# Optimization experiments

Measured on AMD Instinct MI355X. Metric: run time of the kernel, lower is better.

Reference implementation:

```python
import jax, jax.numpy as jnp
import numpy as np

B = 256   # batch size; must equal N for the module's final broadcast to be valid
N = 256   # num feature vectors per sample
D = 1024  # feature dim
S = 1024  # state dim


def setup_inputs() -> dict:
    key = jax.random.key(0)
    k1, k2, k3, k4 = jax.random.split(key, 4)
    return {
        "feature_vectors": jax.random.normal(k1, (B, N, D), dtype=jnp.float32),
        "state_output": jax.random.normal(k2, (B, S), dtype=jnp.float32),
        # tf.random_normal_initializer default stddev=0.05
        "Q": 0.05 * jax.random.normal(k3, (S, S), dtype=jnp.float32),
        "K": 0.05 * jax.random.normal(k4, (S, N), dtype=jnp.float32),
    }


def reference(feature_vectors, state_output, Q, K):
    # Loop body: ((Q @ state^T)^T @ K) @ feature_vectors[i]
    # (Q @ state^T)^T == state @ Q^T  -> [B, S]
    A = state_output @ Q.T            # [B, S]
    M = A @ K                         # [B, N]
    # stack over i: W[i, b, d] = sum_n M[b, n] * FV[i, n, d]
    W = jnp.einsum('bn,ind->ibd', M, feature_vectors)   # [B, B, D]
    W = jax.nn.softmax(W, axis=-1)
    # broadcast multiply [B, B, D] * [B, N(=B), D], sum over axis=1
    context_vector = jnp.sum(W * feature_vectors, axis=1)  # [B, D]
    return (context_vector, W)
```

## Files before the change

### kernel.cpp

```cpp
#include <hip/hip_runtime.h>


typedef _Float16 half8 __attribute__((ext_vector_type(8)));
typedef float floatx16 __attribute__((ext_vector_type(16)));

static __device__ __forceinline__ void split_f32(float x, _Float16& hi, _Float16& lo) {
    _Float16 h = (_Float16)x;
    hi = h;
    lo = (_Float16)(x - (float)h);
}

template <bool BT>
__global__ __launch_bounds__(256, 2) void gemm_splitk(
    const float* __restrict__ Ag, const float* __restrict__ Bg,
    float* __restrict__ Cf, int Kdim, int Ndim, int KC)
{
    __shared__ __align__(16) _Float16 AsHi[4 * 64 * 8];
    __shared__ __align__(16) _Float16 AsLo[4 * 64 * 8];
    __shared__ __align__(16) _Float16 BsHi[4 * 64 * 8];
    __shared__ __align__(16) _Float16 BsLo[4 * 64 * 8];

    const int tid  = threadIdx.x;
    const int lane = tid & 63;
    const int wave = tid >> 6;
    const int wy = wave >> 1, wx = wave & 1;
    const int l31 = lane & 31, l5 = lane >> 5;
    const int m0 = blockIdx.y * 64, n0 = blockIdx.x * 64;
    const int kt0 = (blockIdx.z * KC) >> 5;

    floatx16 acc;
#pragma unroll
    for (int j = 0; j < 16; ++j) acc[j] = 0.0f;

    const int sA_m  = tid >> 2;
    const int sA_kg = tid & 3;
    const int sB_n  = tid & 63;
    const int sB_kg = tid >> 6;

    const int nkt = KC / 32;
#pragma unroll 1
    for (int kt2 = 0; kt2 < nkt; ++kt2) {
        const int kt = kt0 + kt2;
        __syncthreads();
        {
            const float* src = Ag + (size_t)(m0 + sA_m) * Kdim + kt * 32 + sA_kg * 8;
            half8 hi, lo;
#pragma unroll
            for (int j = 0; j < 8; ++j) {
                _Float16 h, l;
                split_f32(src[j], h, l);
                hi[j] = h; lo[j] = l;
            }
            *(half8*)&AsHi[(sA_kg * 64 + sA_m) * 8] = hi;
            *(half8*)&AsLo[(sA_kg * 64 + sA_m) * 8] = lo;
        }
        if constexpr (BT) {
            const float* src = Bg + (size_t)(n0 + sA_m) * Kdim + kt * 32 + sA_kg * 8;
            half8 hi, lo;
#pragma unroll
            for (int j = 0; j < 8; ++j) {
                _Float16 h, l;
                split_f32(src[j], h, l);
                hi[j] = h; lo[j] = l;
            }
            *(half8*)&BsHi[(sA_kg * 64 + sA_m) * 8] = hi;
            *(half8*)&BsLo[(sA_kg * 64 + sA_m) * 8] = lo;
        } else {
            const float* src = Bg + (size_t)(kt * 32 + sB_kg * 8) * Ndim + n0 + sB_n;
            half8 hi, lo;
#pragma unroll
            for (int j = 0; j < 8; ++j) {
                _Float16 h, l;
                split_f32(src[(size_t)j * Ndim], h, l);
                hi[j] = h; lo[j] = l;
            }
            *(half8*)&BsHi[(sB_kg * 64 + sB_n) * 8] = hi;
            *(half8*)&BsLo[(sB_kg * 64 + sB_n) * 8] = lo;
        }
        __syncthreads();
#pragma unroll
        for (int ks = 0; ks < 2; ++ks) {
            const int kg = ks * 2 + l5;
            const half8 ah = *(half8*)&AsHi[(kg * 64 + wy * 32 + l31) * 8];
            const half8 al = *(half8*)&AsLo[(kg * 64 + wy * 32 + l31) * 8];
            const half8 bh = *(half8*)&BsHi[(kg * 64 + wx * 32 + l31) * 8];
            const half8 bl = *(half8*)&BsLo[(kg * 64 + wx * 32 + l31) * 8];
            acc = __builtin_amdgcn_mfma_f32_32x32x16_f16(ah, bh, acc, 0, 0, 0);
            acc = __builtin_amdgcn_mfma_f32_32x32x16_f16(ah, bl, acc, 0, 0, 0);
            acc = __builtin_amdgcn_mfma_f32_32x32x16_f16(al, bh, acc, 0, 0, 0);
        }
    }

#pragma unroll
    for (int reg = 0; reg < 16; ++reg) {
        const int row = m0 + wy * 32 + (reg & 3) + 8 * (reg >> 2) + 4 * l5;
        const int col = n0 + wx * 32 + l31;
        atomicAdd(&Cf[(size_t)row * Ndim + col], acc[reg]);
    }
}

static __device__ __forceinline__ int bs_swz(int byte_off) {
    return byte_off ^ (((byte_off >> 7) & 7) << 4);
}

__global__ __launch_bounds__(512, 2) void fused_attn(
    const float* __restrict__ FV, const float* __restrict__ Mf,
    float* __restrict__ ctx, float* __restrict__ Wout)
{
    __shared__ __align__(16) _Float16 AsHi[2 * 64 * 8];
    __shared__ __align__(16) _Float16 AsLo[2 * 64 * 8];
    __shared__ __align__(16) _Float16 Bs[2 * 1024 * 8];
    __shared__ __align__(16) float red1[64 * 4];
    __shared__ __align__(16) float red2[64 * 4];

    const int tid  = threadIdx.x;
    const int lane = tid & 63;
    const int wave = tid >> 6;
    const int wx = wave & 3;
    const int wy = wave >> 2;
    const int l31 = lane & 31, l5 = lane >> 5;

    const int w   = blockIdx.x;
    const int xcd = w & 7;
    const int k   = w >> 3;
    const int i   = (xcd << 5) + (k >> 2);
    const int bt  = k & 3;

    const float* __restrict__ FVi = FV + (size_t)i * 256 * 1024;

    floatx16 acc[8];
#pragma unroll
    for (int nt = 0; nt < 8; ++nt)
#pragma unroll
        for (int j = 0; j < 16; ++j) acc[nt][j] = 0.0f;

    const int am = tid >> 1, akg = tid & 1;

    const int n8 = tid >> 8;
    const int c0 = (tid & 255) * 4;

    float4 pv4[8];
    float4 pa0, pa1;
    {
        const float* src = FVi + (size_t)(n8 * 8) * 1024 + c0;
#pragma unroll
        for (int r = 0; r < 8; ++r) pv4[r] = *(const float4*)(src + (size_t)r * 1024);
    }
    if (tid < 128) {
        const float* ap = Mf + (size_t)(bt * 64 + am) * 256 + akg * 8;
        pa0 = *(const float4*)(ap);
        pa1 = *(const float4*)(ap + 4);
    }

#pragma unroll 1
    for (int kt = 0; kt < 16; ++kt) {
        __syncthreads();
        if (tid < 128) {
            half8 hi, lo;
#pragma unroll
            for (int j = 0; j < 4; ++j) {
                _Float16 h, l;
                split_f32((&pa0.x)[j], h, l);
                hi[j] = h; lo[j] = l;
            }
#pragma unroll
            for (int j = 0; j < 4; ++j) {
                _Float16 h, l;
                split_f32((&pa1.x)[j], h, l);
                hi[4 + j] = h; lo[4 + j] = l;
            }
            *(half8*)&AsHi[(akg * 64 + am) * 8] = hi;
            *(half8*)&AsLo[(akg * 64 + am) * 8] = lo;
        }
#pragma unroll
        for (int j = 0; j < 4; ++j) {
            half8 h;
#pragma unroll
            for (int r = 0; r < 8; ++r) h[r] = (_Float16)((&pv4[r].x)[j]);
            const int byte_off = (n8 * 1024 + c0 + j) * 16;
            *(half8*)((char*)Bs + bs_swz(byte_off)) = h;
        }
        __syncthreads();
        if (kt + 1 < 16) {
            const float* src = FVi + (size_t)((kt + 1) * 16 + n8 * 8) * 1024 + c0;
#pragma unroll
            for (int r = 0; r < 8; ++r) pv4[r] = *(const float4*)(src + (size_t)r * 1024);
            if (tid < 128) {
                const float* ap = Mf + (size_t)(bt * 64 + am) * 256 + (kt + 1) * 16 + akg * 8;
                pa0 = *(const float4*)(ap);
                pa1 = *(const float4*)(ap + 4);
            }
        }
        const half8 ah = *(half8*)&AsHi[(l5 * 64 + wy * 32 + l31) * 8];
        const half8 al = *(half8*)&AsLo[(l5 * 64 + wy * 32 + l31) * 8];
#pragma unroll
        for (int nt = 0; nt < 8; ++nt) {
            const int byte_off = (l5 * 1024 + wx * 256 + nt * 32 + l31) * 16;
            const half8 b = *(const half8*)((const char*)Bs + bs_swz(byte_off));
            acc[nt] = __builtin_amdgcn_mfma_f32_32x32x16_f16(ah, b, acc[nt], 0, 0, 0);
            acc[nt] = __builtin_amdgcn_mfma_f32_32x32x16_f16(al, b, acc[nt], 0, 0, 0);
        }
    }

    float st[16];
#pragma unroll
    for (int reg = 0; reg < 16; ++reg) {
        float v = acc[0][reg];
#pragma unroll
        for (int nt = 1; nt < 8; ++nt) v = fmaxf(v, acc[nt][reg]);
#pragma unroll
        for (int off = 1; off < 32; off <<= 1) v = fmaxf(v, __shfl_xor(v, off));
        st[reg] = v;
    }
    if (l31 == 0) {
#pragma unroll
        for (int reg = 0; reg < 16; ++reg) {
            const int row = wy * 32 + (reg & 3) + 8 * (reg >> 2) + 4 * l5;
            red1[row * 4 + wx] = st[reg];
        }
    }
    __syncthreads();
    float rmax[16];
#pragma unroll
    for (int reg = 0; reg < 16; ++reg) {
        const int row = wy * 32 + (reg & 3) + 8 * (reg >> 2) + 4 * l5;
        const float4 m4 = *(const float4*)&red1[row * 4];
        rmax[reg] = fmaxf(fmaxf(m4.x, m4.y), fmaxf(m4.z, m4.w));
    }
#pragma unroll
    for (int reg = 0; reg < 16; ++reg) {
        float s = 0.0f;
#pragma unroll
        for (int nt = 0; nt < 8; ++nt) {
            const float p = __expf(acc[nt][reg] - rmax[reg]);
            acc[nt][reg] = p;
            s += p;
        }
#pragma unroll
        for (int off = 1; off < 32; off <<= 1) s += __shfl_xor(s, off);
        st[reg] = s;
    }
    if (l31 == 0) {
#pragma unroll
        for (int reg = 0; reg < 16; ++reg) {
            const int row = wy * 32 + (reg & 3) + 8 * (reg >> 2) + 4 * l5;
            red2[row * 4 + wx] = st[reg];
        }
    }
    __syncthreads();
    float inv[16];
#pragma unroll
    for (int reg = 0; reg < 16; ++reg) {
        const int row = wy * 32 + (reg & 3) + 8 * (reg >> 2) + 4 * l5;
        const float4 s4 = *(const float4*)&red2[row * 4];
        inv[reg] = 1.0f / (s4.x + s4.y + s4.z + s4.w);
    }

    float csum[8];
#pragma unroll
    for (int nt = 0; nt < 8; ++nt) csum[nt] = 0.0f;

    const int rowbase = bt * 64 + wy * 32;
#pragma unroll
    for (int nt = 0; nt < 8; ++nt) {
        const int col = wx * 256 + nt * 32 + l31;
#pragma unroll
        for (int reg = 0; reg < 16; ++reg) {
            const int row = (reg & 3) + 8 * (reg >> 2) + 4 * l5;
            const float wv = acc[nt][reg] * inv[reg];
            Wout[((size_t)(i * 256 + rowbase + row)) * 1024 + col] = wv;
            const float fv = FVi[(size_t)(rowbase + row) * 1024 + col];
            csum[nt] += wv * fv;
        }
    }
#pragma unroll
    for (int nt = 0; nt < 8; ++nt) {
        const float v = csum[nt] + __shfl_xor(csum[nt], 32);
        if (l5 == 0)
            atomicAdd(&ctx[(size_t)i * 1024 + wx * 256 + nt * 32 + l31], v);
    }
}

extern "C" void kernel_launch(void* const* d_in, const int* in_sizes, int n_in,
                              void* d_out, int out_size, void* d_ws, size_t ws_size,
                              hipStream_t stream)
{
    const float* FV    = (const float*)d_in[0];
    const float* state = (const float*)d_in[1];
    const float* Q     = (const float*)d_in[2];
    const float* Km    = (const float*)d_in[3];

    float* out = (float*)d_out;
    float* ctx = out;
    float* W   = out + 256 * 1024;

    char* ws = (char*)d_ws;
    float* A1 = (float*)ws;
    float* Mf = (float*)(ws + (1 << 20));

    (void)hipMemsetAsync(ws, 0, (1 << 20) + (1 << 18), stream);
    (void)hipMemsetAsync(ctx, 0, 256 * 1024 * sizeof(float), stream);

    gemm_splitk<true><<<dim3(16, 4, 8), 256, 0, stream>>>(
        state, Q, A1, 1024, 1024, 128);

    gemm_splitk<false><<<dim3(4, 4, 16), 256, 0, stream>>>(
        A1, Km, Mf, 1024, 256, 64);

    fused_attn<<<dim3(1024), 512, 0, stream>>>(FV, Mf, ctx, W);
}
```

Measured before the change: 588.0 us.

## Double fused attention block to 1024 threads with 16 waves and smaller per-wave tiles

```diff
diff --git a/kernel.cpp b/kernel.cpp
--- a/kernel.cpp
+++ b/kernel.cpp
@@ -2,6 +2,7 @@
 
 
 typedef _Float16 half8 __attribute__((ext_vector_type(8)));
+typedef _Float16 half4 __attribute__((ext_vector_type(4)));
 typedef float floatx16 __attribute__((ext_vector_type(16)));
 
 static __device__ __forceinline__ void split_f32(float x, _Float16& hi, _Float16& lo) {
@@ -103,21 +104,21 @@
     return byte_off ^ (((byte_off >> 7) & 7) << 4);
 }
 
-__global__ __launch_bounds__(512, 2) void fused_attn(
+__global__ __launch_bounds__(1024, 4) void fused_attn(
     const float* __restrict__ FV, const float* __restrict__ Mf,
     float* __restrict__ ctx, float* __restrict__ Wout)
 {
     __shared__ __align__(16) _Float16 AsHi[2 * 64 * 8];
     __shared__ __align__(16) _Float16 AsLo[2 * 64 * 8];
     __shared__ __align__(16) _Float16 Bs[2 * 1024 * 8];
-    __shared__ __align__(16) float red1[64 * 4];
-    __shared__ __align__(16) float red2[64 * 4];
+    __shared__ __align__(16) float red1[64 * 8];
+    __shared__ __align__(16) float red2[64 * 8];
 
     const int tid  = threadIdx.x;
     const int lane = tid & 63;
     const int wave = tid >> 6;
-    const int wx = wave & 3;
-    const int wy = wave >> 2;
+    const int wx = wave & 7;
+    const int wy = wave >> 3;
     const int l31 = lane & 31, l5 = lane >> 5;
 
     const int w   = blockIdx.x;
@@ -128,24 +129,22 @@
 
     const float* __restrict__ FVi = FV + (size_t)i * 256 * 1024;
 
-    floatx16 acc[8];
-#pragma unroll
-    for (int nt = 0; nt < 8; ++nt)
+    floatx16 acc[4];
+#pragma unroll
+    for (int nt = 0; nt < 4; ++nt)
 #pragma unroll
         for (int j = 0; j < 16; ++j) acc[nt][j] = 0.0f;
 
     const int am = tid >> 1, akg = tid & 1;
 
-    const int n8 = tid >> 8;
-    const int c0 = (tid & 255) * 4;
-
-    float4 pv4[8];
+    const int ng = tid >> 8;
+    const int dq = tid & 255;
+
+    float4 pv[4];
     float4 pa0, pa1;
-    {
-        const float* src = FVi + (size_t)(n8 * 8) * 1024 + c0;
-#pragma unroll
-        for (int r = 0; r < 8; ++r) pv4[r] = *(const float4*)(src + (size_t)r * 1024);
-    }
+#pragma unroll
+    for (int r = 0; r < 4; ++r)
+        pv[r] = *(const float4*)(FVi + (size_t)(ng * 4 + r) * 1024 + dq * 4);
     if (tid < 128) {
         const float* ap = Mf + (size_t)(bt * 64 + am) * 256 + akg * 8;
         pa0 = *(const float4*)(ap);
@@ -174,17 +173,17 @@
         }
 #pragma unroll
         for (int j = 0; j < 4; ++j) {
-            half8 h;
-#pragma unroll
-            for (int r = 0; r < 8; ++r) h[r] = (_Float16)((&pv4[r].x)[j]);
-            const int byte_off = (n8 * 1024 + c0 + j) * 16;
-            *(half8*)((char*)Bs + bs_swz(byte_off)) = h;
+            half4 h;
+#pragma unroll
+            for (int r = 0; r < 4; ++r) h[r] = (_Float16)((&pv[r].x)[j]);
+            const int byte_off = ((ng >> 1) * 1024 + dq * 4 + j) * 16 + (ng & 1) * 8;
+            *(half4*)((char*)Bs + bs_swz(byte_off)) = h;
         }
         __syncthreads();
         if (kt + 1 < 16) {
-            const float* src = FVi + (size_t)((kt + 1) * 16 + n8 * 8) * 1024 + c0;
-#pragma unroll
-            for (int r = 0; r < 8; ++r) pv4[r] = *(const float4*)(src + (size_t)r * 1024);
+#pragma unroll
+            for (int r = 0; r < 4; ++r)
+                pv[r] = *(const float4*)(FVi + (size_t)((kt + 1) * 16 + ng * 4 + r) * 1024 + dq * 4);
             if (tid < 128) {
                 const float* ap = Mf + (size_t)(bt * 64 + am) * 256 + (kt + 1) * 16 + akg * 8;
                 pa0 = *(const float4*)(ap);
@@ -194,90 +193,72 @@
         const half8 ah = *(half8*)&AsHi[(l5 * 64 + wy * 32 + l31) * 8];
         const half8 al = *(half8*)&AsLo[(l5 * 64 + wy * 32 + l31) * 8];
 #pragma unroll
-        for (int nt = 0; nt < 8; ++nt) {
-            const int byte_off = (l5 * 1024 + wx * 256 + nt * 32 + l31) * 16;
+        for (int nt = 0; nt < 4; ++nt) {
+            const int byte_off = (l5 * 1024 + wx * 128 + nt * 32 + l31) * 16;
             const half8 b = *(const half8*)((const char*)Bs + bs_swz(byte_off));
             acc[nt] = __builtin_amdgcn_mfma_f32_32x32x16_f16(ah, b, acc[nt], 0, 0, 0);
             acc[nt] = __builtin_amdgcn_mfma_f32_32x32x16_f16(al, b, acc[nt], 0, 0, 0);
         }
     }
 
-    float st[16];
 #pragma unroll
     for (int reg = 0; reg < 16; ++reg) {
         float v = acc[0][reg];
 #pragma unroll
-        for (int nt = 1; nt < 8; ++nt) v = fmaxf(v, acc[nt][reg]);
+        for (int nt = 1; nt < 4; ++nt) v = fmaxf(v, acc[nt][reg]);
 #pragma unroll
         for (int off = 1; off < 32; off <<= 1) v = fmaxf(v, __shfl_xor(v, off));
-        st[reg] = v;
-    }
-    if (l31 == 0) {
-#pragma unroll
-        for (int reg = 0; reg < 16; ++reg) {
+        if (l31 == 0) {
             const int row = wy * 32 + (reg & 3) + 8 * (reg >> 2) + 4 * l5;
-            red1[row * 4 + wx] = st[reg];
+            red1[row * 8 + wx] = v;
         }
     }
     __syncthreads();
-    float rmax[16];
 #pragma unroll
     for (int reg = 0; reg < 16; ++reg) {
         const int row = wy * 32 + (reg & 3) + 8 * (reg >> 2) + 4 * l5;
-        const float4 m4 = *(const float4*)&red1[row * 4];
-        rmax[reg] = fmaxf(fmaxf(m4.x, m4.y), fmaxf(m4.z, m4.w));
-    }
-#pragma unroll
-    for (int reg = 0; reg < 16; ++reg) {
+        const float4 a4 = *(const float4*)&red1[row * 8];
+        const float4 b4 = *(const float4*)&red1[row * 8 + 4];
+        const float rmax = fmaxf(fmaxf(fmaxf(a4.x, a4.y), fmaxf(a4.z, a4.w)),
+                                 fmaxf(fmaxf(b4.x, b4.y), fmaxf(b4.z, b4.w)));
         float s = 0.0f;
 #pragma unroll
-        for (int nt = 0; nt < 8; ++nt) {
-            const float p = __expf(acc[nt][reg] - rmax[reg]);
+        for (int nt = 0; nt < 4; ++nt) {
+            const float p = __expf(acc[nt][reg] - rmax);
             acc[nt][reg] = p;
             s += p;
         }
 #pragma unroll
         for (int off = 1; off < 32; off <<= 1) s += __shfl_xor(s, off);
-        st[reg] = s;
-    }
-    if (l31 == 0) {
-#pragma unroll
-        for (int reg = 0; reg < 16; ++reg) {
-            const int row = wy * 32 + (reg & 3) + 8 * (reg >> 2) + 4 * l5;
-            red2[row * 4 + wx] = st[reg];
-        }
+        if (l31 == 0) red2[row * 8 + wx] = s;
     }
     __syncthreads();
-    float inv[16];
-#pragma unroll
-    for (int reg = 0; reg < 16; ++reg) {
-        const int row = wy * 32 + (reg & 3) + 8 * (reg >> 2) + 4 * l5;
-        const float4 s4 = *(const float4*)&red2[row * 4];
-        inv[reg] = 1.0f / (s4.x + s4.y + s4.z + s4.w);
-    }
-
-    float csum[8];
-#pragma unroll
-    for (int nt = 0; nt < 8; ++nt) csum[nt] = 0.0f;
+
+    float csum[4];
+#pragma unroll
+    for (int nt = 0; nt < 4; ++nt) csum[nt] = 0.0f;
 
     const int rowbase = bt * 64 + wy * 32;
 #pragma unroll
-    for (int nt = 0; nt < 8; ++nt) {
-        const int col = wx * 256 + nt * 32 + l31;
-#pragma unroll
-        for (int reg = 0; reg < 16; ++reg) {
-            const int row = (reg & 3) + 8 * (reg >> 2) + 4 * l5;
-            const float wv = acc[nt][reg] * inv[reg];
+    for (int reg = 0; reg < 16; ++reg) {
+        const int row = (reg & 3) + 8 * (reg >> 2) + 4 * l5;
+        const float4 a4 = *(const float4*)&red2[(wy * 32 + row) * 8];
+        const float4 b4 = *(const float4*)&red2[(wy * 32 + row) * 8 + 4];
+        const float inv = 1.0f / (a4.x + a4.y + a4.z + a4.w + b4.x + b4.y + b4.z + b4.w);
+#pragma unroll
+        for (int nt = 0; nt < 4; ++nt) {
+            const int col = wx * 128 + nt * 32 + l31;
+            const float wv = acc[nt][reg] * inv;
             Wout[((size_t)(i * 256 + rowbase + row)) * 1024 + col] = wv;
             const float fv = FVi[(size_t)(rowbase + row) * 1024 + col];
             csum[nt] += wv * fv;
         }
     }
 #pragma unroll
-    for (int nt = 0; nt < 8; ++nt) {
+    for (int nt = 0; nt < 4; ++nt) {
         const float v = csum[nt] + __shfl_xor(csum[nt], 32);
         if (l5 == 0)
-            atomicAdd(&ctx[(size_t)i * 1024 + wx * 256 + nt * 32 + l31], v);
+            atomicAdd(&ctx[(size_t)i * 1024 + wx * 128 + nt * 32 + l31], v);
     }
 }
 
@@ -307,5 +288,5 @@
     gemm_splitk<false><<<dim3(4, 4, 16), 256, 0, stream>>>(
         A1, Km, Mf, 1024, 256, 64);
 
-    fused_attn<<<dim3(1024), 512, 0, stream>>>(FV, Mf, ctx, W);
-}
+    fused_attn<<<dim3(1024), 1024, 0, stream>>>(FV, Mf, ctx, W);
+}
```

New measurement: 585.7 us. Within noise of the previous version (-0.4%).

## Pre-convert feature vectors to fp16 in a pass fused with the first GEMM

Applied to the files above, without the earlier changes.

```diff
diff --git a/kernel.cpp b/kernel.cpp
--- a/kernel.cpp
+++ b/kernel.cpp
@@ -2,6 +2,7 @@
 
 
 typedef _Float16 half8 __attribute__((ext_vector_type(8)));
+typedef _Float16 half4 __attribute__((ext_vector_type(4)));
 typedef float floatx16 __attribute__((ext_vector_type(16)));
 
 static __device__ __forceinline__ void split_f32(float x, _Float16& hi, _Float16& lo) {
@@ -10,10 +11,10 @@
     lo = (_Float16)(x - (float)h);
 }
 
-template <bool BT>
-__global__ __launch_bounds__(256, 2) void gemm_splitk(
+template <bool BT, bool SPLITK>
+__device__ __forceinline__ void gemm_body(
     const float* __restrict__ Ag, const float* __restrict__ Bg,
-    float* __restrict__ Cf, int Kdim, int Ndim, int KC)
+    float* __restrict__ Cf, int Kdim, int Ndim, int KC, int bx, int by, int bz)
 {
     __shared__ __align__(16) _Float16 AsHi[4 * 64 * 8];
     __shared__ __align__(16) _Float16 AsLo[4 * 64 * 8];
@@ -25,8 +26,8 @@
     const int wave = tid >> 6;
     const int wy = wave >> 1, wx = wave & 1;
     const int l31 = lane & 31, l5 = lane >> 5;
-    const int m0 = blockIdx.y * 64, n0 = blockIdx.x * 64;
-    const int kt0 = (blockIdx.z * KC) >> 5;
+    const int m0 = by * 64, n0 = bx * 64;
+    const int kt0 = (bz * KC) >> 5;
 
     floatx16 acc;
 #pragma unroll
@@ -95,8 +96,47 @@
     for (int reg = 0; reg < 16; ++reg) {
         const int row = m0 + wy * 32 + (reg & 3) + 8 * (reg >> 2) + 4 * l5;
         const int col = n0 + wx * 32 + l31;
-        atomicAdd(&Cf[(size_t)row * Ndim + col], acc[reg]);
-    }
+        if constexpr (SPLITK) atomicAdd(&Cf[(size_t)row * Ndim + col], acc[reg]);
+        else                  Cf[(size_t)row * Ndim + col] = acc[reg];
+    }
+}
+
+template <bool BT>
+__global__ __launch_bounds__(256, 2) void gemm_splitk(
+    const float* __restrict__ Ag, const float* __restrict__ Bg,
+    float* __restrict__ Cf, int Kdim, int Ndim, int KC)
+{
+    gemm_body<BT, true>(Ag, Bg, Cf, Kdim, Ndim, KC,
+                        blockIdx.x, blockIdx.y, blockIdx.z);
+}
+
+__device__ __forceinline__ void fv16_copy_body(
+    const float* __restrict__ FV, _Float16* __restrict__ T, int i, int tile, int z)
+{
+    const size_t base = (size_t)i * 262144 + (size_t)tile * 16384 + (size_t)z * 2048;
+    const float* src = FV + base;
+    _Float16* dst = T + base;
+    const int tid = threadIdx.x;
+#pragma unroll
+    for (int j = 0; j < 2; ++j) {
+        const float4 v = *(const float4*)(src + (size_t)(j * 256 + tid) * 4);
+        half4 h;
+        h[0] = (_Float16)v.x; h[1] = (_Float16)v.y;
+        h[2] = (_Float16)v.z; h[3] = (_Float16)v.w;
+        *(half4*)(dst + (size_t)(j * 256 + tid) * 4) = h;
+    }
+}
+
+__global__ __launch_bounds__(256, 2) void gemm1_plus_copy(
+    const float* __restrict__ state, const float* __restrict__ Q,
+    float* __restrict__ A1,
+    const float* __restrict__ FV, _Float16* __restrict__ T)
+{
+    if (blockIdx.y < 4)
+        gemm_body<true, true>(state, Q, A1, 1024, 1024, 128,
+                              blockIdx.x, blockIdx.y, blockIdx.z);
+    else
+        fv16_copy_body(FV, T, blockIdx.y - 4, blockIdx.x, blockIdx.z);
 }
 
 static __device__ __forceinline__ int bs_swz(int byte_off) {
@@ -104,7 +144,7 @@
 }
 
 __global__ __launch_bounds__(512, 2) void fused_attn(
-    const float* __restrict__ FV, const float* __restrict__ Mf,
+    const _Float16* __restrict__ FV16, const float* __restrict__ Mf,
     float* __restrict__ ctx, float* __restrict__ Wout)
 {
     __shared__ __align__(16) _Float16 AsHi[2 * 64 * 8];
@@ -126,7 +166,7 @@
     const int i   = (xcd << 5) + (k >> 2);
     const int bt  = k & 3;
 
-    const float* __restrict__ FVi = FV + (size_t)i * 256 * 1024;
+    const _Float16* __restrict__ Fi = FV16 + (size_t)i * 262144;
 
     floatx16 acc[8];
 #pragma unroll
@@ -139,12 +179,12 @@
     const int n8 = tid >> 8;
     const int c0 = (tid & 255) * 4;
 
-    float4 pv4[8];
+    half4 pv[8];
     float4 pa0, pa1;
     {
-        const float* src = FVi + (size_t)(n8 * 8) * 1024 + c0;
-#pragma unroll
-        for (int r = 0; r < 8; ++r) pv4[r] = *(const float4*)(src + (size_t)r * 1024);
+        const _Float16* src = Fi + (size_t)(n8 * 8) * 1024 + c0;
+#pragma unroll
+        for (int r = 0; r < 8; ++r) pv[r] = *(const half4*)(src + (size_t)r * 1024);
     }
     if (tid < 128) {
         const float* ap = Mf + (size_t)(bt * 64 + am) * 256 + akg * 8;
@@ -176,15 +216,15 @@
         for (int j = 0; j < 4; ++j) {
             half8 h;
 #pragma unroll
-            for (int r = 0; r < 8; ++r) h[r] = (_Float16)((&pv4[r].x)[j]);
+            for (int r = 0; r < 8; ++r) h[r] = pv[r][j];
             const int byte_off = (n8 * 1024 + c0 + j) * 16;
             *(half8*)((char*)Bs + bs_swz(byte_off)) = h;
         }
         __syncthreads();
         if (kt + 1 < 16) {
-            const float* src = FVi + (size_t)((kt + 1) * 16 + n8 * 8) * 1024 + c0;
-#pragma unroll
-            for (int r = 0; r < 8; ++r) pv4[r] = *(const float4*)(src + (size_t)r * 1024);
+            const _Float16* src = Fi + (size_t)((kt + 1) * 16 + n8 * 8) * 1024 + c0;
+#pragma unroll
+            for (int r = 0; r < 8; ++r) pv[r] = *(const half4*)(src + (size_t)r * 1024);
             if (tid < 128) {
                 const float* ap = Mf + (size_t)(bt * 64 + am) * 256 + (kt + 1) * 16 + akg * 8;
                 pa0 = *(const float4*)(ap);
@@ -269,7 +309,7 @@
             const int row = (reg & 3) + 8 * (reg >> 2) + 4 * l5;
             const float wv = acc[nt][reg] * inv[reg];
             Wout[((size_t)(i * 256 + rowbase + row)) * 1024 + col] = wv;
-            const float fv = FVi[(size_t)(rowbase + row) * 1024 + col];
+            const float fv = (float)Fi[(size_t)(rowbase + row) * 1024 + col];
             csum[nt] += wv * fv;
         }
     }
@@ -295,17 +335,17 @@
     float* W   = out + 256 * 1024;
 
     char* ws = (char*)d_ws;
-    float* A1 = (float*)ws;
-    float* Mf = (float*)(ws + (1 << 20));
+    float*    A1 = (float*)ws;
+    float*    Mf = (float*)(ws + (1 << 20));
+    _Float16* T  = (_Float16*)(ws + (1 << 20) + (1 << 18));
 
     (void)hipMemsetAsync(ws, 0, (1 << 20) + (1 << 18), stream);
     (void)hipMemsetAsync(ctx, 0, 256 * 1024 * sizeof(float), stream);
 
-    gemm_splitk<true><<<dim3(16, 4, 8), 256, 0, stream>>>(
-        state, Q, A1, 1024, 1024, 128);
+    gemm1_plus_copy<<<dim3(16, 260, 8), 256, 0, stream>>>(state, Q, A1, FV, T);
 
     gemm_splitk<false><<<dim3(4, 4, 16), 256, 0, stream>>>(
         A1, Km, Mf, 1024, 256, 64);
 
-    fused_attn<<<dim3(1024), 512, 0, stream>>>(FV, Mf, ctx, W);
-}
+    fused_attn<<<dim3(1024), 512, 0, stream>>>(T, Mf, ctx, W);
+}
```

Result: slower. 625.6 us (+6.4%).
